# Performance work log

Hardware: AMD Instinct MI355X
Metric: run time of the kernel (lower is better)

The kernel has to match this reference:

```python
import jax, jax.numpy as jnp
import numpy as np

B, L, D_PAIR, N_HEAD = 1, 320, 128, 4
EPS = 1e-5


def setup_inputs() -> dict:
    key = jax.random.key(0)
    ks = jax.random.split(key, 8)
    s = 0.05  # ~xavier scale for fan_in=128
    return {
        "pair": jax.random.normal(ks[0], (B, L, L, D_PAIR), jnp.float32),
        "norm_w": jnp.ones((D_PAIR,), jnp.float32),
        "norm_b": jnp.zeros((D_PAIR,), jnp.float32),
        "Wq": jax.random.normal(ks[1], (D_PAIR, D_PAIR), jnp.float32) * s,
        "Wk": jax.random.normal(ks[2], (D_PAIR, D_PAIR), jnp.float32) * s,
        "Wv": jax.random.normal(ks[3], (D_PAIR, D_PAIR), jnp.float32) * s,
        "Wg": jax.random.normal(ks[4], (D_PAIR, D_PAIR), jnp.float32) * s,
        "bg": jnp.zeros((D_PAIR,), jnp.float32),
        "Wo": jax.random.normal(ks[5], (D_PAIR, D_PAIR), jnp.float32) * s,
        "bo": jnp.zeros((D_PAIR,), jnp.float32),
        "Wb": jax.random.normal(ks[6], (N_HEAD, D_PAIR), jnp.float32) * s,
    }


def reference(pair, norm_w, norm_b, Wq, Wk, Wv, Wg, bg, Wo, bo, Wb):
    # Triangle attention, mode='start' (no permute). pair: (B, L, L, D)
    Bs, Ls, _, D = pair.shape
    H = Wb.shape[0]
    Dh = D // H
    scale = Dh ** -0.5

    # LayerNorm (fp32, matches torch eps=1e-5)
    mu = jnp.mean(pair, axis=-1, keepdims=True)
    var = jnp.var(pair, axis=-1, keepdims=True)
    x = (pair - mu) * jax.lax.rsqrt(var + EPS) * norm_w + norm_b

    def heads(y):
        # (B,L,L,D) -> (B,L,H,L,Dh): attention runs along the second L axis per row i
        return y.reshape(Bs, Ls, Ls, H, Dh).transpose(0, 1, 3, 2, 4)

    Q = heads(x @ Wq.T)
    K = heads(x @ Wk.T)
    V = heads(x @ Wv.T)
    g = heads(jax.nn.sigmoid(x @ Wg.T + bg))

    attn = jnp.einsum('blhid,blhjd->blhij', Q, K) * scale  # (B,L,H,L,L)
    # bias from RAW pair (pre-norm), projected to heads, broadcast over query index i
    bias = (pair @ Wb.T).transpose(0, 1, 3, 2)[:, :, :, None, :]  # (B,L,H,1,L)
    attn = jax.nn.softmax(attn + bias, axis=-1)

    out = jnp.einsum('blhij,blhjd->blhid', attn, V)  # (B,L,H,L,Dh)
    out = (g * out).transpose(0, 1, 3, 2, 4).reshape(Bs, Ls, Ls, D)
    return pair + out @ Wo.T + bo
```

## Files before the change

kernel.cpp:

```cpp
#include <hip/hip_runtime.h>

typedef unsigned short u16;
typedef unsigned int u32;
typedef __attribute__((ext_vector_type(8))) short bf16x8;
typedef __attribute__((ext_vector_type(4))) float f32x4;
typedef __attribute__((ext_vector_type(2))) unsigned int u32x2;

#define LOG2E 1.4426950408889634f

__device__ __forceinline__ u16 f2bf(float f) {
    u32 u = __float_as_uint(f);
    u += 0x7fffu + ((u >> 16) & 1u);
    return (u16)(u >> 16);
}
__device__ __forceinline__ float bf2f(u16 s) {
    return __uint_as_float(((u32)s) << 16);
}
__device__ __forceinline__ u32 pk_bf_trunc(float hi, float lo) {
    return __builtin_amdgcn_perm(__float_as_uint(hi), __float_as_uint(lo), 0x07060302u);
}

__global__ void wconv_kernel(const float* __restrict__ Wq, const float* __restrict__ Wk,
                             const float* __restrict__ Wv, const float* __restrict__ Wg,
                             const float* __restrict__ Wo, u16* __restrict__ wbf) {
    int idx = blockIdx.x * blockDim.x + threadIdx.x;
    wbf[0 * 16384 + idx] = f2bf(Wq[idx]);
    wbf[1 * 16384 + idx] = f2bf(Wk[idx]);
    wbf[2 * 16384 + idx] = f2bf(Wv[idx]);
    wbf[3 * 16384 + idx] = f2bf(Wg[idx]);
    wbf[4 * 16384 + idx] = f2bf(Wo[idx]);
}

#define KS_OFF 9216
#define VTS_OFF 22016
#define PB_W 1152

__global__ __launch_bounds__(512, 4)
void attn_kernel(const float* __restrict__ pair,
                 const float* __restrict__ norm_w,
                 const float* __restrict__ norm_b,
                 const float* __restrict__ bg,
                 const float* __restrict__ Wb,
                 const u16* __restrict__ wbf,
                 u16* __restrict__ Obf,
                 u16* __restrict__ Gg) {
    const int l = blockIdx.x >> 2;
    const int h = blockIdx.x & 3;
    const int tid = threadIdx.x;
    const int wave = tid >> 6;
    const int lane = tid & 63;
    const int i_lo = lane & 15;
    const int q = lane >> 4;

    __shared__ __align__(16) u16 smem[32512];
    __shared__ __align__(16) float biasLds[320];
    __shared__ __align__(16) float wls[384];

    if (tid < 96) {
        int a = tid >> 5;
        int t = tid & 31;
        const float* src = (a == 0) ? norm_w : (a == 1) ? norm_b : (Wb + h * 128);
        f32x4 v = *(const f32x4*)(src + t * 4);
        *(f32x4*)&wls[a * 128 + t * 4] = v;
    }

    float bg0 = bg[h * 32 + i_lo];
    float bg1 = bg[h * 32 + 16 + i_lo];

    __syncthreads();

    const int row_g = tid >> 3;
    const int c8 = tid & 7;
    const int wrow = (wave & 3) * 16;
    const int nth_flip = wave >> 2;

    u32 qkeep[3][4];

#pragma unroll 1
    for (int t = 0; t < 5; ++t) {
        const int j0 = t * 64;
        const float* prow = pair + ((size_t)(l * 320 + j0 + row_g)) * 128 + c8 * 16;
        f32x4 pr[4];
#pragma unroll
        for (int u = 0; u < 4; ++u) pr[u] = *(const f32x4*)(prow + u * 4);

        float s = 0.f, s2 = 0.f, bd = 0.f;
#pragma unroll
        for (int u = 0; u < 4; ++u) {
            f32x4 p = pr[u];
            f32x4 wb4 = *(const f32x4*)&wls[256 + c8 * 16 + u * 4];
            s += p[0] + p[1] + p[2] + p[3];
            s2 += p[0] * p[0] + p[1] * p[1] + p[2] * p[2] + p[3] * p[3];
            bd += p[0] * wb4[0] + p[1] * wb4[1] + p[2] * wb4[2] + p[3] * wb4[3];
        }
        s += __shfl_xor(s, 1);   s += __shfl_xor(s, 2);   s += __shfl_xor(s, 4);
        s2 += __shfl_xor(s2, 1); s2 += __shfl_xor(s2, 2); s2 += __shfl_xor(s2, 4);
        bd += __shfl_xor(bd, 1); bd += __shfl_xor(bd, 2); bd += __shfl_xor(bd, 4);
        float mu = s * 0.0078125f;
        float var = s2 * 0.0078125f - mu * mu;
        float rs = rsqrtf(var + 1e-5f);

        __syncthreads();
#pragma unroll
        for (int u = 0; u < 4; ++u) {
            f32x4 p = pr[u];
            f32x4 w4 = *(const f32x4*)&wls[0 + c8 * 16 + u * 4];
            f32x4 b4 = *(const f32x4*)&wls[128 + c8 * 16 + u * 4];
            ushort4 xv;
            xv.x = f2bf((p[0] - mu) * rs * w4[0] + b4[0]);
            xv.y = f2bf((p[1] - mu) * rs * w4[1] + b4[1]);
            xv.z = f2bf((p[2] - mu) * rs * w4[2] + b4[2]);
            xv.w = f2bf((p[3] - mu) * rs * w4[3] + b4[3]);
            *(ushort4*)&smem[row_g * 136 + c8 * 16 + u * 4] = xv;
        }
        if (c8 == 0) biasLds[j0 + row_g] = bd * LOG2E;
        __syncthreads();

        const int nth = (t & 1) ^ nth_flip;
        f32x4 acc[4];
#pragma unroll
        for (int n2 = 0; n2 < 4; ++n2) acc[n2] = (f32x4){0.f, 0.f, 0.f, 0.f};
#pragma unroll
        for (int kc = 0; kc < 4; ++kc) {
            bf16x8 a = *(const bf16x8*)&smem[(wrow + i_lo) * 136 + kc * 32 + q * 8];
#pragma unroll
            for (int n2 = 0; n2 < 4; ++n2) {
                int nt = nth * 4 + n2;
                bf16x8 wf = *(const bf16x8*)&wbf[(nt >> 1) * 16384 +
                                                 (h * 32 + (nt & 1) * 16 + i_lo) * 128 + kc * 32 + q * 8];
                acc[n2] = __builtin_amdgcn_mfma_f32_16x16x32_bf16(a, wf, acc[n2], 0, 0, 0);
            }
        }
        const int jrow = j0 + wrow + q * 4;
        if (nth == 0) {
            const int ti = t >> 1;
#pragma unroll
            for (int dd = 0; dd < 2; ++dd)
#pragma unroll
                for (int rr = 0; rr < 2; ++rr)
                    qkeep[ti][dd * 2 + rr] =
                        (u32)f2bf(acc[dd][rr * 2]) | ((u32)f2bf(acc[dd][rr * 2 + 1]) << 16);
#pragma unroll
            for (int n2 = 2; n2 < 4; ++n2)
#pragma unroll
                for (int r = 0; r < 4; ++r)
                    smem[KS_OFF + (jrow + r) * 40 + (n2 & 1) * 16 + i_lo] = f2bf(acc[n2][r]);
        } else {
#pragma unroll
            for (int n2 = 0; n2 < 2; ++n2)
#pragma unroll
                for (int r = 0; r < 4; ++r)
                    smem[VTS_OFF + (n2 * 16 + i_lo) * 328 + jrow + r] = f2bf(acc[n2][r]);
#pragma unroll
            for (int n2 = 2; n2 < 4; ++n2)
#pragma unroll
                for (int r = 0; r < 4; ++r) {
                    float z = acc[n2][r] + ((n2 & 1) ? bg1 : bg0);
                    float g = 1.0f / (1.0f + exp2f(-z * LOG2E));
                    Gg[((size_t)((l * 4 + h) * 320 + jrow + r)) * 32 + (n2 & 1) * 16 + i_lo] = f2bf(g);
                }
        }
    }
    __syncthreads();

    const float SC = 0.17677669529663687f * LOG2E;
    const f32x4 zero4 = {0.f, 0.f, 0.f, 0.f};
    u16* pb = smem + wave * PB_W;
    const int nstrip = (wave < 4) ? 3 : 2;
#pragma unroll 1
    for (int t2 = 0; t2 < nstrip; ++t2) {
        const int i0 = (wave + 8 * t2) * 16;
#pragma unroll
        for (int dd = 0; dd < 2; ++dd)
#pragma unroll
            for (int rr = 0; rr < 2; ++rr) {
                u32 v = qkeep[t2][dd * 2 + rr];
                pb[(q * 4 + rr * 2) * 40 + dd * 16 + i_lo] = (u16)v;
                pb[(q * 4 + rr * 2 + 1) * 40 + dd * 16 + i_lo] = (u16)(v >> 16);
            }
        bf16x8 qf = *(const bf16x8*)&pb[i_lo * 40 + q * 8];

        f32x4 oacc[2];
        oacc[0] = zero4; oacc[1] = zero4;
        float sum = 0.f;
#pragma unroll 1
        for (int c = 0; c < 5; ++c) {
            f32x4 sc4[4];
#pragma unroll
            for (int jt = 0; jt < 4; ++jt) {
                bf16x8 kf = *(const bf16x8*)&smem[KS_OFF + (c * 64 + jt * 16 + i_lo) * 40 + q * 8];
                sc4[jt] = __builtin_amdgcn_mfma_f32_16x16x32_bf16(kf, qf, zero4, 0, 0, 0);
            }
#pragma unroll
            for (int jt = 0; jt < 4; ++jt) {
                f32x4 b4 = *(const f32x4*)&biasLds[c * 64 + jt * 16 + q * 4];
#pragma unroll
                for (int r = 0; r < 4; ++r) {
                    float p = exp2f(sc4[jt][r] * SC + b4[r]);
                    sc4[jt][r] = p;
                    sum += p;
                }
            }
#pragma unroll
            for (int jt = 0; jt < 4; ++jt) {
                u32x2 pk;
                pk.x = pk_bf_trunc(sc4[jt][1], sc4[jt][0]);
                pk.y = pk_bf_trunc(sc4[jt][3], sc4[jt][2]);
                *(u32x2*)&pb[i_lo * 72 + jt * 16 + q * 4] = pk;
            }
#pragma unroll
            for (int kt2 = 0; kt2 < 2; ++kt2) {
                bf16x8 pf = *(const bf16x8*)&pb[i_lo * 72 + kt2 * 32 + q * 8];
#pragma unroll
                for (int mt = 0; mt < 2; ++mt) {
                    bf16x8 vf = *(const bf16x8*)&smem[VTS_OFF + (mt * 16 + i_lo) * 328 +
                                                      c * 64 + kt2 * 32 + q * 8];
                    oacc[mt] = __builtin_amdgcn_mfma_f32_16x16x32_bf16(vf, pf, oacc[mt], 0, 0, 0);
                }
            }
        }
        sum += __shfl_xor(sum, 16);
        sum += __shfl_xor(sum, 32);
        float rinv = 1.0f / sum;
#pragma unroll
        for (int mt = 0; mt < 2; ++mt) {
            u32x2 pk;
            pk.x = pk_bf_trunc(oacc[mt][1] * rinv, oacc[mt][0] * rinv);
            pk.y = pk_bf_trunc(oacc[mt][3] * rinv, oacc[mt][2] * rinv);
            *(u32x2*)&Obf[((size_t)(l * 320 + i0 + i_lo)) * 128 + h * 32 + mt * 16 + q * 4] = pk;
        }
    }
}

__global__ __launch_bounds__(256)
void outproj_kernel(const float* __restrict__ pair,
                    const float* __restrict__ bo,
                    const u16* __restrict__ Obf,
                    const u16* __restrict__ Gg,
                    const u16* __restrict__ wbf,
                    float* __restrict__ out) {
    const int tid = threadIdx.x;
    const int wave = tid >> 6;
    const int lane = tid & 63;
    const int i_lo = lane & 15;
    const int q = lane >> 4;
    const int blk = blockIdx.x;
    const int mrow = blk * 64 + wave * 16;
    const int lidx = blk / 5;
    const int irow = mrow - lidx * 320 + i_lo;
    const u16* Wo = wbf + 4 * 16384;

    bf16x8 of[4];
#pragma unroll
    for (int kc = 0; kc < 4; ++kc) {
        union { bf16x8 v; u32 u[4]; } A, G, R;
        A.v = *(const bf16x8*)&Obf[((size_t)(mrow + i_lo)) * 128 + kc * 32 + q * 8];
        G.v = *(const bf16x8*)&Gg[((size_t)((lidx * 4 + kc) * 320 + irow)) * 32 + q * 8];
#pragma unroll
        for (int k4 = 0; k4 < 4; ++k4) {
            float lo = __uint_as_float(A.u[k4] << 16) * __uint_as_float(G.u[k4] << 16);
            float hi = __uint_as_float(A.u[k4] & 0xffff0000u) * __uint_as_float(G.u[k4] & 0xffff0000u);
            R.u[k4] = pk_bf_trunc(hi, lo);
        }
        of[kc] = R.v;
    }

    f32x4 acc[8];
#pragma unroll
    for (int nt = 0; nt < 8; ++nt) acc[nt] = (f32x4){0.f, 0.f, 0.f, 0.f};
#pragma unroll
    for (int nt = 0; nt < 8; ++nt) {
#pragma unroll
        for (int kc = 0; kc < 4; ++kc) {
            bf16x8 wf = *(const bf16x8*)&Wo[(nt * 16 + i_lo) * 128 + kc * 32 + q * 8];
            acc[nt] = __builtin_amdgcn_mfma_f32_16x16x32_bf16(wf, of[kc], acc[nt], 0, 0, 0);
        }
    }
#pragma unroll
    for (int nt = 0; nt < 8; ++nt) {
        size_t idx = ((size_t)(mrow + i_lo)) * 128 + nt * 16 + q * 4;
        f32x4 p4 = *(const f32x4*)&pair[idx];
        f32x4 b4 = *(const f32x4*)&bo[nt * 16 + q * 4];
        f32x4 o4;
        o4[0] = acc[nt][0] + p4[0] + b4[0];
        o4[1] = acc[nt][1] + p4[1] + b4[1];
        o4[2] = acc[nt][2] + p4[2] + b4[2];
        o4[3] = acc[nt][3] + p4[3] + b4[3];
        *(f32x4*)&out[idx] = o4;
    }
}

extern "C" void kernel_launch(void* const* d_in, const int* in_sizes, int n_in,
                              void* d_out, int out_size, void* d_ws, size_t ws_size,
                              hipStream_t stream) {
    const float* pair   = (const float*)d_in[0];
    const float* norm_w = (const float*)d_in[1];
    const float* norm_b = (const float*)d_in[2];
    const float* Wq     = (const float*)d_in[3];
    const float* Wk     = (const float*)d_in[4];
    const float* Wv     = (const float*)d_in[5];
    const float* Wg     = (const float*)d_in[6];
    const float* bg     = (const float*)d_in[7];
    const float* Wo     = (const float*)d_in[8];
    const float* bo     = (const float*)d_in[9];
    const float* Wb     = (const float*)d_in[10];

    u16* wbf = (u16*)d_ws;
    u16* Obf = wbf + 5 * 16384;
    u16* Gg  = Obf + (size_t)102400 * 128;
    float* out = (float*)d_out;

    wconv_kernel<<<64, 256, 0, stream>>>(Wq, Wk, Wv, Wg, Wo, wbf);
    attn_kernel<<<320 * 4, 512, 0, stream>>>(pair, norm_w, norm_b, bg, Wb, wbf, Obf, Gg);
    outproj_kernel<<<1600, 256, 0, stream>>>(pair, bo, Obf, Gg, wbf, out);
}
```

Before: 294.5 us.

## Process two heads per block, fold LayerNorm affine into weights, coalesce output stores

Each attention block now handles two heads for one row l, so the pair-row LayerNorm pass and global pair reads happen half as often. Q, K, V and G for both heads are kept in a larger LDS buffer. The LayerNorm scale is folded into the bf16 projection weights, and the bias terms (norm_b·W plus bg) are precomputed into a constant vector added after the MFMA. The output projection stages accumulators through LDS so the residual add and stores are row-contiguous and coalesced. The cost is much more LDS per block and lower occupancy (launch bounds change from 4 to 2 blocks), plus a small extra precompute in the weight-conversion kernel.

```diff
diff --git a/kernel.cpp b/kernel.cpp
--- a/kernel.cpp
+++ b/kernel.cpp
@@ -22,59 +22,80 @@
 
 __global__ void wconv_kernel(const float* __restrict__ Wq, const float* __restrict__ Wk,
                              const float* __restrict__ Wv, const float* __restrict__ Wg,
-                             const float* __restrict__ Wo, u16* __restrict__ wbf) {
-    int idx = blockIdx.x * blockDim.x + threadIdx.x;
-    wbf[0 * 16384 + idx] = f2bf(Wq[idx]);
-    wbf[1 * 16384 + idx] = f2bf(Wk[idx]);
-    wbf[2 * 16384 + idx] = f2bf(Wv[idx]);
-    wbf[3 * 16384 + idx] = f2bf(Wg[idx]);
-    wbf[4 * 16384 + idx] = f2bf(Wo[idx]);
-}
-
-#define KS_OFF 9216
-#define VTS_OFF 22016
+                             const float* __restrict__ Wo, const float* __restrict__ norm_w,
+                             const float* __restrict__ norm_b, const float* __restrict__ bg,
+                             u16* __restrict__ wbf, float* __restrict__ cvec) {
+    int b = blockIdx.x;
+    if (b < 64) {
+        int idx = b * 256 + threadIdx.x;
+        float w = norm_w[idx & 127];
+        wbf[0 * 16384 + idx] = f2bf(Wq[idx] * w);
+        wbf[1 * 16384 + idx] = f2bf(Wk[idx] * w);
+        wbf[2 * 16384 + idx] = f2bf(Wv[idx] * w);
+        wbf[3 * 16384 + idx] = f2bf(Wg[idx] * w);
+        wbf[4 * 16384 + idx] = f2bf(Wo[idx]);
+    } else {
+        int m = b - 64;
+        int n = threadIdx.x;
+        if (n < 128) {
+            const float* W = (m == 0) ? Wq : (m == 1) ? Wk : (m == 2) ? Wv : Wg;
+            float c = 0.f;
+#pragma unroll
+            for (int k4 = 0; k4 < 32; ++k4) {
+                f32x4 bb = *(const f32x4*)&norm_b[k4 * 4];
+                f32x4 ww = *(const f32x4*)&W[n * 128 + k4 * 4];
+                c += bb[0] * ww[0] + bb[1] * ww[1] + bb[2] * ww[2] + bb[3] * ww[3];
+            }
+            if (m == 3) c += bg[n];
+            cvec[m * 128 + n] = c;
+        }
+    }
+}
+
 #define PB_W 1152
-
-__global__ __launch_bounds__(512, 4)
+#define QALL_OFF 9216
+#define KS_OFF 29696
+#define VTS_OFF 55296
+
+__global__ __launch_bounds__(512, 2)
 void attn_kernel(const float* __restrict__ pair,
-                 const float* __restrict__ norm_w,
-                 const float* __restrict__ norm_b,
-                 const float* __restrict__ bg,
                  const float* __restrict__ Wb,
                  const u16* __restrict__ wbf,
+                 const float* __restrict__ cvec,
                  u16* __restrict__ Obf,
                  u16* __restrict__ Gg) {
-    const int l = blockIdx.x >> 2;
-    const int h = blockIdx.x & 3;
+    const int l = blockIdx.x >> 1;
+    const int hp = blockIdx.x & 1;
     const int tid = threadIdx.x;
     const int wave = tid >> 6;
     const int lane = tid & 63;
     const int i_lo = lane & 15;
     const int q = lane >> 4;
 
-    __shared__ __align__(16) u16 smem[32512];
-    __shared__ __align__(16) float biasLds[320];
-    __shared__ __align__(16) float wls[384];
-
-    if (tid < 96) {
-        int a = tid >> 5;
-        int t = tid & 31;
-        const float* src = (a == 0) ? norm_w : (a == 1) ? norm_b : (Wb + h * 128);
-        f32x4 v = *(const f32x4*)(src + t * 4);
-        *(f32x4*)&wls[a * 128 + t * 4] = v;
-    }
-
-    float bg0 = bg[h * 32 + i_lo];
-    float bg1 = bg[h * 32 + 16 + i_lo];
-
-    __syncthreads();
+    __shared__ __align__(16) u16 smem[76288];
+    __shared__ __align__(16) float biasLds[640];
 
     const int row_g = tid >> 3;
     const int c8 = tid & 7;
     const int wrow = (wave & 3) * 16;
     const int nth_flip = wave >> 2;
 
-    u32 qkeep[3][4];
+    f32x4 wbv[2][4];
+#pragma unroll
+    for (int hh = 0; hh < 2; ++hh)
+#pragma unroll
+        for (int u = 0; u < 4; ++u)
+            wbv[hh][u] = *(const f32x4*)&Wb[(hp * 2 + hh) * 128 + c8 * 16 + u * 4];
+
+    float cQ[4], cK[4], cV[4], cG[4];
+#pragma unroll
+    for (int e = 0; e < 4; ++e) {
+        int n = (hp * 2 + (e >> 1)) * 32 + (e & 1) * 16 + i_lo;
+        cQ[e] = cvec[0 * 128 + n];
+        cK[e] = cvec[1 * 128 + n];
+        cV[e] = cvec[2 * 128 + n];
+        cG[e] = cvec[3 * 128 + n];
+    }
 
 #pragma unroll 1
     for (int t = 0; t < 5; ++t) {
@@ -84,18 +105,20 @@
 #pragma unroll
         for (int u = 0; u < 4; ++u) pr[u] = *(const f32x4*)(prow + u * 4);
 
-        float s = 0.f, s2 = 0.f, bd = 0.f;
+        float s = 0.f, s2 = 0.f, bd0 = 0.f, bd1 = 0.f;
 #pragma unroll
         for (int u = 0; u < 4; ++u) {
             f32x4 p = pr[u];
-            f32x4 wb4 = *(const f32x4*)&wls[256 + c8 * 16 + u * 4];
             s += p[0] + p[1] + p[2] + p[3];
             s2 += p[0] * p[0] + p[1] * p[1] + p[2] * p[2] + p[3] * p[3];
-            bd += p[0] * wb4[0] + p[1] * wb4[1] + p[2] * wb4[2] + p[3] * wb4[3];
-        }
-        s += __shfl_xor(s, 1);   s += __shfl_xor(s, 2);   s += __shfl_xor(s, 4);
-        s2 += __shfl_xor(s2, 1); s2 += __shfl_xor(s2, 2); s2 += __shfl_xor(s2, 4);
-        bd += __shfl_xor(bd, 1); bd += __shfl_xor(bd, 2); bd += __shfl_xor(bd, 4);
+            f32x4 w0 = wbv[0][u], w1 = wbv[1][u];
+            bd0 += p[0] * w0[0] + p[1] * w0[1] + p[2] * w0[2] + p[3] * w0[3];
+            bd1 += p[0] * w1[0] + p[1] * w1[1] + p[2] * w1[2] + p[3] * w1[3];
+        }
+        s += __shfl_xor(s, 1);     s += __shfl_xor(s, 2);     s += __shfl_xor(s, 4);
+        s2 += __shfl_xor(s2, 1);   s2 += __shfl_xor(s2, 2);   s2 += __shfl_xor(s2, 4);
+        bd0 += __shfl_xor(bd0, 1); bd0 += __shfl_xor(bd0, 2); bd0 += __shfl_xor(bd0, 4);
+        bd1 += __shfl_xor(bd1, 1); bd1 += __shfl_xor(bd1, 2); bd1 += __shfl_xor(bd1, 4);
         float mu = s * 0.0078125f;
         float var = s2 * 0.0078125f - mu * mu;
         float rs = rsqrtf(var + 1e-5f);
@@ -104,61 +127,67 @@
 #pragma unroll
         for (int u = 0; u < 4; ++u) {
             f32x4 p = pr[u];
-            f32x4 w4 = *(const f32x4*)&wls[0 + c8 * 16 + u * 4];
-            f32x4 b4 = *(const f32x4*)&wls[128 + c8 * 16 + u * 4];
             ushort4 xv;
-            xv.x = f2bf((p[0] - mu) * rs * w4[0] + b4[0]);
-            xv.y = f2bf((p[1] - mu) * rs * w4[1] + b4[1]);
-            xv.z = f2bf((p[2] - mu) * rs * w4[2] + b4[2]);
-            xv.w = f2bf((p[3] - mu) * rs * w4[3] + b4[3]);
+            xv.x = f2bf((p[0] - mu) * rs);
+            xv.y = f2bf((p[1] - mu) * rs);
+            xv.z = f2bf((p[2] - mu) * rs);
+            xv.w = f2bf((p[3] - mu) * rs);
             *(ushort4*)&smem[row_g * 136 + c8 * 16 + u * 4] = xv;
         }
-        if (c8 == 0) biasLds[j0 + row_g] = bd * LOG2E;
+        if (c8 == 0) {
+            biasLds[j0 + row_g] = bd0 * LOG2E;
+            biasLds[320 + j0 + row_g] = bd1 * LOG2E;
+        }
         __syncthreads();
 
         const int nth = (t & 1) ^ nth_flip;
-        f32x4 acc[4];
-#pragma unroll
-        for (int n2 = 0; n2 < 4; ++n2) acc[n2] = (f32x4){0.f, 0.f, 0.f, 0.f};
+        const int m0 = nth * 2;
+        f32x4 acc[8];
+#pragma unroll
+        for (int e = 0; e < 8; ++e) acc[e] = (f32x4){0.f, 0.f, 0.f, 0.f};
 #pragma unroll
         for (int kc = 0; kc < 4; ++kc) {
             bf16x8 a = *(const bf16x8*)&smem[(wrow + i_lo) * 136 + kc * 32 + q * 8];
 #pragma unroll
-            for (int n2 = 0; n2 < 4; ++n2) {
-                int nt = nth * 4 + n2;
-                bf16x8 wf = *(const bf16x8*)&wbf[(nt >> 1) * 16384 +
-                                                 (h * 32 + (nt & 1) * 16 + i_lo) * 128 + kc * 32 + q * 8];
-                acc[n2] = __builtin_amdgcn_mfma_f32_16x16x32_bf16(a, wf, acc[n2], 0, 0, 0);
-            }
-        }
+            for (int e = 0; e < 4; ++e) {
+                int n = (hp * 2 + (e >> 1)) * 32 + (e & 1) * 16 + i_lo;
+                bf16x8 wfa = *(const bf16x8*)&wbf[m0 * 16384 + n * 128 + kc * 32 + q * 8];
+                acc[e] = __builtin_amdgcn_mfma_f32_16x16x32_bf16(a, wfa, acc[e], 0, 0, 0);
+                bf16x8 wfb = *(const bf16x8*)&wbf[(m0 + 1) * 16384 + n * 128 + kc * 32 + q * 8];
+                acc[4 + e] = __builtin_amdgcn_mfma_f32_16x16x32_bf16(a, wfb, acc[4 + e], 0, 0, 0);
+            }
+        }
+        const int strip = t * 4 + (wave & 3);
         const int jrow = j0 + wrow + q * 4;
         if (nth == 0) {
-            const int ti = t >> 1;
-#pragma unroll
-            for (int dd = 0; dd < 2; ++dd)
-#pragma unroll
-                for (int rr = 0; rr < 2; ++rr)
-                    qkeep[ti][dd * 2 + rr] =
-                        (u32)f2bf(acc[dd][rr * 2]) | ((u32)f2bf(acc[dd][rr * 2 + 1]) << 16);
-#pragma unroll
-            for (int n2 = 2; n2 < 4; ++n2)
+#pragma unroll
+            for (int e = 0; e < 4; ++e) {
+                int head = e >> 1, half = e & 1;
+                int qb = QALL_OFF + (strip * 2 + head) * 512;
 #pragma unroll
                 for (int r = 0; r < 4; ++r)
-                    smem[KS_OFF + (jrow + r) * 40 + (n2 & 1) * 16 + i_lo] = f2bf(acc[n2][r]);
+                    smem[qb + (q * 4 + r) * 32 + half * 16 + i_lo] = f2bf(acc[e][r] + cQ[e]);
+#pragma unroll
+                for (int r = 0; r < 4; ++r)
+                    smem[KS_OFF + head * 12800 + (jrow + r) * 40 + half * 16 + i_lo] =
+                        f2bf(acc[4 + e][r] + cK[e]);
+            }
         } else {
 #pragma unroll
-            for (int n2 = 0; n2 < 2; ++n2)
+            for (int e = 0; e < 4; ++e) {
+                int head = e >> 1, half = e & 1;
 #pragma unroll
                 for (int r = 0; r < 4; ++r)
-                    smem[VTS_OFF + (n2 * 16 + i_lo) * 328 + jrow + r] = f2bf(acc[n2][r]);
-#pragma unroll
-            for (int n2 = 2; n2 < 4; ++n2)
+                    smem[VTS_OFF + head * 10496 + (half * 16 + i_lo) * 328 + jrow + r] =
+                        f2bf(acc[e][r] + cV[e]);
 #pragma unroll
                 for (int r = 0; r < 4; ++r) {
-                    float z = acc[n2][r] + ((n2 & 1) ? bg1 : bg0);
+                    float z = acc[4 + e][r] + cG[e];
                     float g = 1.0f / (1.0f + exp2f(-z * LOG2E));
-                    Gg[((size_t)((l * 4 + h) * 320 + jrow + r)) * 32 + (n2 & 1) * 16 + i_lo] = f2bf(g);
+                    Gg[((size_t)((l * 4 + hp * 2 + head) * 320 + jrow + r)) * 32 +
+                       half * 16 + i_lo] = f2bf(g);
                 }
+            }
         }
     }
     __syncthreads();
@@ -166,19 +195,13 @@
     const float SC = 0.17677669529663687f * LOG2E;
     const f32x4 zero4 = {0.f, 0.f, 0.f, 0.f};
     u16* pb = smem + wave * PB_W;
-    const int nstrip = (wave < 4) ? 3 : 2;
 #pragma unroll 1
-    for (int t2 = 0; t2 < nstrip; ++t2) {
-        const int i0 = (wave + 8 * t2) * 16;
-#pragma unroll
-        for (int dd = 0; dd < 2; ++dd)
-#pragma unroll
-            for (int rr = 0; rr < 2; ++rr) {
-                u32 v = qkeep[t2][dd * 2 + rr];
-                pb[(q * 4 + rr * 2) * 40 + dd * 16 + i_lo] = (u16)v;
-                pb[(q * 4 + rr * 2 + 1) * 40 + dd * 16 + i_lo] = (u16)(v >> 16);
-            }
-        bf16x8 qf = *(const bf16x8*)&pb[i_lo * 40 + q * 8];
+    for (int t2 = 0; t2 < 5; ++t2) {
+        const int g = wave + 8 * t2;
+        const int strip = g >> 1;
+        const int hh = g & 1;
+        const int i0 = strip * 16;
+        bf16x8 qf = *(const bf16x8*)&smem[QALL_OFF + g * 512 + i_lo * 32 + q * 8];
 
         f32x4 oacc[2];
         oacc[0] = zero4; oacc[1] = zero4;
@@ -188,12 +211,13 @@
             f32x4 sc4[4];
 #pragma unroll
             for (int jt = 0; jt < 4; ++jt) {
-                bf16x8 kf = *(const bf16x8*)&smem[KS_OFF + (c * 64 + jt * 16 + i_lo) * 40 + q * 8];
+                bf16x8 kf = *(const bf16x8*)&smem[KS_OFF + hh * 12800 +
+                                                  (c * 64 + jt * 16 + i_lo) * 40 + q * 8];
                 sc4[jt] = __builtin_amdgcn_mfma_f32_16x16x32_bf16(kf, qf, zero4, 0, 0, 0);
             }
 #pragma unroll
             for (int jt = 0; jt < 4; ++jt) {
-                f32x4 b4 = *(const f32x4*)&biasLds[c * 64 + jt * 16 + q * 4];
+                f32x4 b4 = *(const f32x4*)&biasLds[hh * 320 + c * 64 + jt * 16 + q * 4];
 #pragma unroll
                 for (int r = 0; r < 4; ++r) {
                     float p = exp2f(sc4[jt][r] * SC + b4[r]);
@@ -213,8 +237,9 @@
                 bf16x8 pf = *(const bf16x8*)&pb[i_lo * 72 + kt2 * 32 + q * 8];
 #pragma unroll
                 for (int mt = 0; mt < 2; ++mt) {
-                    bf16x8 vf = *(const bf16x8*)&smem[VTS_OFF + (mt * 16 + i_lo) * 328 +
-                                                      c * 64 + kt2 * 32 + q * 8];
+                    bf16x8 vf = *(const bf16x8*)&smem[VTS_OFF + hh * 10496 +
+                                                      (mt * 16 + i_lo) * 328 + c * 64 +
+                                                      kt2 * 32 + q * 8];
                     oacc[mt] = __builtin_amdgcn_mfma_f32_16x16x32_bf16(vf, pf, oacc[mt], 0, 0, 0);
                 }
             }
@@ -227,7 +252,8 @@
             u32x2 pk;
             pk.x = pk_bf_trunc(oacc[mt][1] * rinv, oacc[mt][0] * rinv);
             pk.y = pk_bf_trunc(oacc[mt][3] * rinv, oacc[mt][2] * rinv);
-            *(u32x2*)&Obf[((size_t)(l * 320 + i0 + i_lo)) * 128 + h * 32 + mt * 16 + q * 4] = pk;
+            *(u32x2*)&Obf[((size_t)(l * 320 + i0 + i_lo)) * 128 +
+                          (hp * 2 + hh) * 32 + mt * 16 + q * 4] = pk;
         }
     }
 }
@@ -250,6 +276,8 @@
     const int irow = mrow - lidx * 320 + i_lo;
     const u16* Wo = wbf + 4 * 16384;
 
+    __shared__ __align__(16) float ot[4][16 * 133];
+
     bf16x8 of[4];
 #pragma unroll
     for (int kc = 0; kc < 4; ++kc) {
@@ -277,16 +305,31 @@
         }
     }
 #pragma unroll
-    for (int nt = 0; nt < 8; ++nt) {
-        size_t idx = ((size_t)(mrow + i_lo)) * 128 + nt * 16 + q * 4;
-        f32x4 p4 = *(const f32x4*)&pair[idx];
-        f32x4 b4 = *(const f32x4*)&bo[nt * 16 + q * 4];
-        f32x4 o4;
-        o4[0] = acc[nt][0] + p4[0] + b4[0];
-        o4[1] = acc[nt][1] + p4[1] + b4[1];
-        o4[2] = acc[nt][2] + p4[2] + b4[2];
-        o4[3] = acc[nt][3] + p4[3] + b4[3];
-        *(f32x4*)&out[idx] = o4;
+    for (int nt = 0; nt < 8; ++nt)
+        *(f32x4*)&ot[wave][i_lo * 133 + nt * 16 + q * 4] = acc[nt];
+    __syncthreads();
+
+    const int r8 = lane >> 3;
+    const int c8i = lane & 7;
+    f32x4 bo4[4];
+#pragma unroll
+    for (int k = 0; k < 4; ++k) bo4[k] = *(const f32x4*)&bo[k * 32 + c8i * 4];
+#pragma unroll
+    for (int u = 0; u < 2; ++u) {
+        int lr = u * 8 + r8;
+        size_t rbase = ((size_t)(mrow + lr)) * 128;
+#pragma unroll
+        for (int k = 0; k < 4; ++k) {
+            int col = k * 32 + c8i * 4;
+            f32x4 v = *(const f32x4*)&ot[wave][lr * 133 + col];
+            f32x4 p4 = *(const f32x4*)&pair[rbase + col];
+            f32x4 o4;
+            o4[0] = v[0] + p4[0] + bo4[k][0];
+            o4[1] = v[1] + p4[1] + bo4[k][1];
+            o4[2] = v[2] + p4[2] + bo4[k][2];
+            o4[3] = v[3] + p4[3] + bo4[k][3];
+            *(f32x4*)&out[rbase + col] = o4;
+        }
     }
 }
 
@@ -305,12 +348,13 @@
     const float* bo     = (const float*)d_in[9];
     const float* Wb     = (const float*)d_in[10];
 
-    u16* wbf = (u16*)d_ws;
-    u16* Obf = wbf + 5 * 16384;
-    u16* Gg  = Obf + (size_t)102400 * 128;
+    u16* wbf   = (u16*)d_ws;
+    float* cvec = (float*)(wbf + 5 * 16384);
+    u16* Obf   = (u16*)(cvec + 512);
+    u16* Gg    = Obf + (size_t)102400 * 128;
     float* out = (float*)d_out;
 
-    wconv_kernel<<<64, 256, 0, stream>>>(Wq, Wk, Wv, Wg, Wo, wbf);
-    attn_kernel<<<320 * 4, 512, 0, stream>>>(pair, norm_w, norm_b, bg, Wb, wbf, Obf, Gg);
+    wconv_kernel<<<68, 256, 0, stream>>>(Wq, Wk, Wv, Wg, Wo, norm_w, norm_b, bg, wbf, cvec);
+    attn_kernel<<<320 * 2, 512, 0, stream>>>(pair, Wb, wbf, cvec, Obf, Gg);
     outproj_kernel<<<1600, 256, 0, stream>>>(pair, bo, Obf, Gg, wbf, out);
 }
```

Result: slower. 342.3 us (+16.2%).

## Fold LayerNorm affine into projection weights and stage Wo in LDS

Applied to the files above, without the earlier changes.

The LayerNorm scale is folded into the Q/K/V/G weight columns, and the bias (norm_b·W plus bg) into per-output constant vectors computed in the weight-prep kernel. The attention kernel no longer applies the affine per element and drops its parameter LDS staging and the initial barrier. The V-transpose LDS row stride is padded from 328 to 330, likely to reduce bank conflicts. The output projection now uses 512-thread blocks that copy Wo into padded LDS once per block instead of reading it from global memory per wave. Folding changes bf16 rounding slightly, and the larger outproj blocks with 33 KB of LDS may lower occupancy.

```diff
diff --git a/kernel.cpp b/kernel.cpp
--- a/kernel.cpp
+++ b/kernel.cpp
@@ -13,22 +13,40 @@
     u += 0x7fffu + ((u >> 16) & 1u);
     return (u16)(u >> 16);
 }
-__device__ __forceinline__ float bf2f(u16 s) {
-    return __uint_as_float(((u32)s) << 16);
-}
 __device__ __forceinline__ u32 pk_bf_trunc(float hi, float lo) {
     return __builtin_amdgcn_perm(__float_as_uint(hi), __float_as_uint(lo), 0x07060302u);
 }
 
 __global__ void wconv_kernel(const float* __restrict__ Wq, const float* __restrict__ Wk,
                              const float* __restrict__ Wv, const float* __restrict__ Wg,
-                             const float* __restrict__ Wo, u16* __restrict__ wbf) {
-    int idx = blockIdx.x * blockDim.x + threadIdx.x;
-    wbf[0 * 16384 + idx] = f2bf(Wq[idx]);
-    wbf[1 * 16384 + idx] = f2bf(Wk[idx]);
-    wbf[2 * 16384 + idx] = f2bf(Wv[idx]);
-    wbf[3 * 16384 + idx] = f2bf(Wg[idx]);
-    wbf[4 * 16384 + idx] = f2bf(Wo[idx]);
+                             const float* __restrict__ Wo, const float* __restrict__ norm_w,
+                             const float* __restrict__ norm_b, const float* __restrict__ bg,
+                             u16* __restrict__ wbf, float* __restrict__ cvec) {
+    int b = blockIdx.x;
+    if (b < 64) {
+        int idx = b * 256 + threadIdx.x;
+        float w = norm_w[idx & 127];
+        wbf[0 * 16384 + idx] = f2bf(Wq[idx] * w);
+        wbf[1 * 16384 + idx] = f2bf(Wk[idx] * w);
+        wbf[2 * 16384 + idx] = f2bf(Wv[idx] * w);
+        wbf[3 * 16384 + idx] = f2bf(Wg[idx] * w);
+        wbf[4 * 16384 + idx] = f2bf(Wo[idx]);
+    } else {
+        int m = b - 64;
+        int n = threadIdx.x;
+        if (n < 128) {
+            const float* W = (m == 0) ? Wq : (m == 1) ? Wk : (m == 2) ? Wv : Wg;
+            float c = 0.f;
+#pragma unroll
+            for (int k4 = 0; k4 < 32; ++k4) {
+                f32x4 bb = *(const f32x4*)&norm_b[k4 * 4];
+                f32x4 ww = *(const f32x4*)&W[n * 128 + k4 * 4];
+                c += bb[0] * ww[0] + bb[1] * ww[1] + bb[2] * ww[2] + bb[3] * ww[3];
+            }
+            if (m == 3) c += bg[n];
+            cvec[m * 128 + n] = c;
+        }
+    }
 }
 
 #define KS_OFF 9216
@@ -37,11 +55,9 @@
 
 __global__ __launch_bounds__(512, 4)
 void attn_kernel(const float* __restrict__ pair,
-                 const float* __restrict__ norm_w,
-                 const float* __restrict__ norm_b,
-                 const float* __restrict__ bg,
                  const float* __restrict__ Wb,
                  const u16* __restrict__ wbf,
+                 const float* __restrict__ cvec,
                  u16* __restrict__ Obf,
                  u16* __restrict__ Gg) {
     const int l = blockIdx.x >> 2;
@@ -52,27 +68,28 @@
     const int i_lo = lane & 15;
     const int q = lane >> 4;
 
-    __shared__ __align__(16) u16 smem[32512];
+    __shared__ __align__(16) u16 smem[32576];
     __shared__ __align__(16) float biasLds[320];
-    __shared__ __align__(16) float wls[384];
-
-    if (tid < 96) {
-        int a = tid >> 5;
-        int t = tid & 31;
-        const float* src = (a == 0) ? norm_w : (a == 1) ? norm_b : (Wb + h * 128);
-        f32x4 v = *(const f32x4*)(src + t * 4);
-        *(f32x4*)&wls[a * 128 + t * 4] = v;
-    }
-
-    float bg0 = bg[h * 32 + i_lo];
-    float bg1 = bg[h * 32 + 16 + i_lo];
-
-    __syncthreads();
 
     const int row_g = tid >> 3;
     const int c8 = tid & 7;
     const int wrow = (wave & 3) * 16;
     const int nth_flip = wave >> 2;
+
+    f32x4 wbv[4];
+#pragma unroll
+    for (int u = 0; u < 4; ++u)
+        wbv[u] = *(const f32x4*)&Wb[h * 128 + c8 * 16 + u * 4];
+
+    float cQ[2], cK[2], cV[2], cG[2];
+#pragma unroll
+    for (int half = 0; half < 2; ++half) {
+        int n = h * 32 + half * 16 + i_lo;
+        cQ[half] = cvec[0 * 128 + n];
+        cK[half] = cvec[1 * 128 + n];
+        cV[half] = cvec[2 * 128 + n];
+        cG[half] = cvec[3 * 128 + n];
+    }
 
     u32 qkeep[3][4];
 
@@ -88,7 +105,7 @@
 #pragma unroll
         for (int u = 0; u < 4; ++u) {
             f32x4 p = pr[u];
-            f32x4 wb4 = *(const f32x4*)&wls[256 + c8 * 16 + u * 4];
+            f32x4 wb4 = wbv[u];
             s += p[0] + p[1] + p[2] + p[3];
             s2 += p[0] * p[0] + p[1] * p[1] + p[2] * p[2] + p[3] * p[3];
             bd += p[0] * wb4[0] + p[1] * wb4[1] + p[2] * wb4[2] + p[3] * wb4[3];
@@ -104,13 +121,11 @@
 #pragma unroll
         for (int u = 0; u < 4; ++u) {
             f32x4 p = pr[u];
-            f32x4 w4 = *(const f32x4*)&wls[0 + c8 * 16 + u * 4];
-            f32x4 b4 = *(const f32x4*)&wls[128 + c8 * 16 + u * 4];
             ushort4 xv;
-            xv.x = f2bf((p[0] - mu) * rs * w4[0] + b4[0]);
-            xv.y = f2bf((p[1] - mu) * rs * w4[1] + b4[1]);
-            xv.z = f2bf((p[2] - mu) * rs * w4[2] + b4[2]);
-            xv.w = f2bf((p[3] - mu) * rs * w4[3] + b4[3]);
+            xv.x = f2bf((p[0] - mu) * rs);
+            xv.y = f2bf((p[1] - mu) * rs);
+            xv.z = f2bf((p[2] - mu) * rs);
+            xv.w = f2bf((p[3] - mu) * rs);
             *(ushort4*)&smem[row_g * 136 + c8 * 16 + u * 4] = xv;
         }
         if (c8 == 0) biasLds[j0 + row_g] = bd * LOG2E;
@@ -139,23 +154,26 @@
 #pragma unroll
                 for (int rr = 0; rr < 2; ++rr)
                     qkeep[ti][dd * 2 + rr] =
-                        (u32)f2bf(acc[dd][rr * 2]) | ((u32)f2bf(acc[dd][rr * 2 + 1]) << 16);
+                        (u32)f2bf(acc[dd][rr * 2] + cQ[dd]) |
+                        ((u32)f2bf(acc[dd][rr * 2 + 1] + cQ[dd]) << 16);
 #pragma unroll
             for (int n2 = 2; n2 < 4; ++n2)
 #pragma unroll
                 for (int r = 0; r < 4; ++r)
-                    smem[KS_OFF + (jrow + r) * 40 + (n2 & 1) * 16 + i_lo] = f2bf(acc[n2][r]);
+                    smem[KS_OFF + (jrow + r) * 40 + (n2 & 1) * 16 + i_lo] =
+                        f2bf(acc[n2][r] + cK[n2 & 1]);
         } else {
 #pragma unroll
             for (int n2 = 0; n2 < 2; ++n2)
 #pragma unroll
                 for (int r = 0; r < 4; ++r)
-                    smem[VTS_OFF + (n2 * 16 + i_lo) * 328 + jrow + r] = f2bf(acc[n2][r]);
+                    smem[VTS_OFF + (n2 * 16 + i_lo) * 330 + jrow + r] =
+                        f2bf(acc[n2][r] + cV[n2]);
 #pragma unroll
             for (int n2 = 2; n2 < 4; ++n2)
 #pragma unroll
                 for (int r = 0; r < 4; ++r) {
-                    float z = acc[n2][r] + ((n2 & 1) ? bg1 : bg0);
+                    float z = acc[n2][r] + cG[n2 & 1];
                     float g = 1.0f / (1.0f + exp2f(-z * LOG2E));
                     Gg[((size_t)((l * 4 + h) * 320 + jrow + r)) * 32 + (n2 & 1) * 16 + i_lo] = f2bf(g);
                 }
@@ -213,7 +231,7 @@
                 bf16x8 pf = *(const bf16x8*)&pb[i_lo * 72 + kt2 * 32 + q * 8];
 #pragma unroll
                 for (int mt = 0; mt < 2; ++mt) {
-                    bf16x8 vf = *(const bf16x8*)&smem[VTS_OFF + (mt * 16 + i_lo) * 328 +
+                    bf16x8 vf = *(const bf16x8*)&smem[VTS_OFF + (mt * 16 + i_lo) * 330 +
                                                       c * 64 + kt2 * 32 + q * 8];
                     oacc[mt] = __builtin_amdgcn_mfma_f32_16x16x32_bf16(vf, pf, oacc[mt], 0, 0, 0);
                 }
@@ -232,7 +250,7 @@
     }
 }
 
-__global__ __launch_bounds__(256)
+__global__ __launch_bounds__(512, 6)
 void outproj_kernel(const float* __restrict__ pair,
                     const float* __restrict__ bo,
                     const u16* __restrict__ Obf,
@@ -244,17 +262,26 @@
     const int lane = tid & 63;
     const int i_lo = lane & 15;
     const int q = lane >> 4;
-    const int blk = blockIdx.x;
-    const int mrow = blk * 64 + wave * 16;
-    const int lidx = blk / 5;
-    const int irow = mrow - lidx * 320 + i_lo;
+
+    __shared__ __align__(16) u16 WoLds[128 * 132];
     const u16* Wo = wbf + 4 * 16384;
+#pragma unroll
+    for (int it = 0; it < 4; ++it) {
+        int unit = it * 512 + tid;
+        int n = unit >> 4, k8 = unit & 15;
+        *(bf16x8*)&WoLds[n * 132 + k8 * 8] = *(const bf16x8*)&Wo[unit * 8];
+    }
+    __syncthreads();
+
+    const int row0 = blockIdx.x * 128 + wave * 16;
+    const int lidx = row0 / 320;
+    const int irow = row0 - lidx * 320 + i_lo;
 
     bf16x8 of[4];
 #pragma unroll
     for (int kc = 0; kc < 4; ++kc) {
         union { bf16x8 v; u32 u[4]; } A, G, R;
-        A.v = *(const bf16x8*)&Obf[((size_t)(mrow + i_lo)) * 128 + kc * 32 + q * 8];
+        A.v = *(const bf16x8*)&Obf[((size_t)(row0 + i_lo)) * 128 + kc * 32 + q * 8];
         G.v = *(const bf16x8*)&Gg[((size_t)((lidx * 4 + kc) * 320 + irow)) * 32 + q * 8];
 #pragma unroll
         for (int k4 = 0; k4 < 4; ++k4) {
@@ -272,13 +299,13 @@
     for (int nt = 0; nt < 8; ++nt) {
 #pragma unroll
         for (int kc = 0; kc < 4; ++kc) {
-            bf16x8 wf = *(const bf16x8*)&Wo[(nt * 16 + i_lo) * 128 + kc * 32 + q * 8];
+            bf16x8 wf = *(const bf16x8*)&WoLds[(nt * 16 + i_lo) * 132 + kc * 32 + q * 8];
             acc[nt] = __builtin_amdgcn_mfma_f32_16x16x32_bf16(wf, of[kc], acc[nt], 0, 0, 0);
         }
     }
 #pragma unroll
     for (int nt = 0; nt < 8; ++nt) {
-        size_t idx = ((size_t)(mrow + i_lo)) * 128 + nt * 16 + q * 4;
+        size_t idx = ((size_t)(row0 + i_lo)) * 128 + nt * 16 + q * 4;
         f32x4 p4 = *(const f32x4*)&pair[idx];
         f32x4 b4 = *(const f32x4*)&bo[nt * 16 + q * 4];
         f32x4 o4;
@@ -305,12 +332,13 @@
     const float* bo     = (const float*)d_in[9];
     const float* Wb     = (const float*)d_in[10];
 
-    u16* wbf = (u16*)d_ws;
-    u16* Obf = wbf + 5 * 16384;
-    u16* Gg  = Obf + (size_t)102400 * 128;
-    float* out = (float*)d_out;
-
-    wconv_kernel<<<64, 256, 0, stream>>>(Wq, Wk, Wv, Wg, Wo, wbf);
-    attn_kernel<<<320 * 4, 512, 0, stream>>>(pair, norm_w, norm_b, bg, Wb, wbf, Obf, Gg);
-    outproj_kernel<<<1600, 256, 0, stream>>>(pair, bo, Obf, Gg, wbf, out);
-}
+    u16* wbf    = (u16*)d_ws;
+    float* cvec = (float*)(wbf + 5 * 16384);
+    u16* Obf    = (u16*)(cvec + 512);
+    u16* Gg     = Obf + (size_t)102400 * 128;
+    float* out  = (float*)d_out;
+
+    wconv_kernel<<<68, 256, 0, stream>>>(Wq, Wk, Wv, Wg, Wo, norm_w, norm_b, bg, wbf, cvec);
+    attn_kernel<<<320 * 4, 512, 0, stream>>>(pair, Wb, wbf, cvec, Obf, Gg);
+    outproj_kernel<<<800, 512, 0, stream>>>(pair, bo, Obf, Gg, wbf, out);
+}
```

New measurement: 281.1 us. -4.6%, faster.
